# Performance work log

Hardware: AMD Instinct MI355X
Metric: run time of the kernel (lower is better)

## Reference

```python
import jax, jax.numpy as jnp
import numpy as np

NUM_HEADS = 16
NUM_KV_HEADS = 8
FEATURES = 3584
HEAD_DIM = 256
QUERY_SCALAR = 0.0625  # 1/sqrt(head_dim)
SOFT_CAP = 50.0
WINDOW = 1024
K_MASK = -2.3819763e+38
B, T = 1, 2048


def apply_rope(x, positions, head_dim, max_wavelength=10000):
    # x: [B,T,N,H], positions: [B,T]
    fraction = 2.0 * jnp.arange(head_dim // 2, dtype=jnp.float32) / head_dim
    timescale = max_wavelength ** fraction  # [H/2]
    sinusoid = positions[..., None].astype(jnp.float32) / timescale  # [B,T,H/2]
    sinusoid = sinusoid[..., None, :]  # [B,T,1,H/2]
    sin, cos = jnp.sin(sinusoid), jnp.cos(sinusoid)
    first, second = jnp.split(x, 2, axis=-1)
    return jnp.concatenate([first * cos - second * sin, second * cos + first * sin], axis=-1).astype(x.dtype)


def sliding_mask(segment_pos, window, cache_len):
    # cache=None prefill path: total_tokens == cache_len, cache_positions = arange
    cp = jnp.arange(cache_len)[None, None, :]      # [1,1,S]
    sp = segment_pos[:, :, None]                   # [B,T,1]
    return (cp > sp - window) & (cp < sp + window)  # [B,T,S]


def setup_inputs() -> dict:
    key = jax.random.key(0)
    k1, k2, k3, k4 = jax.random.split(key, 4)
    x = jax.random.normal(k1, (B, T, FEATURES), jnp.float32)
    wq = jax.random.normal(k2, (NUM_HEADS, FEATURES, HEAD_DIM), jnp.float32) * 0.02
    wkv = jax.random.normal(k3, (2, NUM_KV_HEADS, FEATURES, HEAD_DIM), jnp.float32) * 0.02
    wo = jax.random.normal(k4, (NUM_HEADS, HEAD_DIM, FEATURES), jnp.float32) * 0.02
    segment_pos = jnp.broadcast_to(jnp.arange(T, dtype=jnp.int32)[None, :], (B, T))
    attn_mask = jnp.broadcast_to(jnp.tril(jnp.ones((T, T), bool))[None], (B, T, T))
    return {"x": x, "segment_pos": segment_pos, "attn_mask": attn_mask, "wq": wq, "wkv": wkv, "wo": wo}


def reference(x, segment_pos, attn_mask, wq, wkv, wo):
    # Projections (GQA path: num_kv_heads != num_heads)
    q = jnp.einsum('BTD,NDH->BTNH', x, wq)            # [B,T,N,H]
    k, v = jnp.einsum('BSD,CKDH->CBSKH', x, wkv)      # each [B,S,K,H]
    q = apply_rope(q, segment_pos, HEAD_DIM) * QUERY_SCALAR
    k = apply_rope(k, segment_pos, HEAD_DIM)
    b, t, n, h = q.shape
    g = n // NUM_KV_HEADS
    qg = q.reshape(b, t, NUM_KV_HEADS, g, h)
    logits = jnp.einsum('BTKGH,BSKH->BTKGS', qg, k).reshape(b, t, n, t)
    # logit soft-capping
    logits = jnp.tanh(logits / SOFT_CAP) * SOFT_CAP
    # sliding-window (LOCAL_SLIDING) combined with causal mask
    mask = attn_mask & sliding_mask(segment_pos, WINDOW, t)
    padded = jnp.where(mask[:, :, None, :], logits, K_MASK)
    probs = jax.nn.softmax(padded, axis=-1).astype(k.dtype)
    pg = probs.reshape(b, t, NUM_KV_HEADS, g, t)
    encoded = jnp.einsum('BTKGS,BSKH->BTKGH', pg, v).reshape(b, t, n, h)
    return jnp.einsum('BTNH,NHD->BTD', encoded, wo)
```

## Files before the change

### kernel.cpp

```cpp
#include <hip/hip_runtime.h>
#include <stdint.h>

typedef unsigned short u16;
typedef __attribute__((ext_vector_type(8))) short short8;
typedef __attribute__((ext_vector_type(4))) float f32x4;

#define SEQ    2048
#define FEAT   3584
#define NHEAD  16
#define HD     256
#define WSLOT  917504

static __device__ __forceinline__ float bf2f(u16 v){
  union { unsigned u; float f; } x; x.u = ((unsigned)v) << 16; return x.f;
}
static __device__ __forceinline__ u16 f2bf(float f){
  union { float f; unsigned u; } x; x.f = f;
  unsigned r = x.u + 0x7fffu + ((x.u >> 16) & 1u);
  return (u16)(r >> 16);
}

static __device__ __forceinline__ void gl_lds16(const u16* g, u16* l){
  __builtin_amdgcn_global_load_lds((const __attribute__((address_space(1))) void*)g,
                                   (__attribute__((address_space(3))) void*)l,
                                   16, 0, 0);
}

__global__ void k_conv_x(const float* __restrict__ x, u16* __restrict__ xb){
  int i = (blockIdx.x * 256 + threadIdx.x) * 4;
  float4 v = *(const float4*)(x + i);
  ushort4 o; o.x = f2bf(v.x); o.y = f2bf(v.y); o.z = f2bf(v.z); o.w = f2bf(v.w);
  *(ushort4*)(xb + i) = o;
}

__global__ void k_rope_tab(const int* __restrict__ sp, float* __restrict__ rc, float* __restrict__ rs){
  int idx = blockIdx.x * 256 + threadIdx.x;
  int t = idx >> 7, i = idx & 127;
  float ts = powf(10000.0f, (float)i * (1.0f / 128.0f));
  float ang = (float)sp[t] / ts;
  float s, c;
  sincosf(ang, &s, &c);
  rc[idx] = c; rs[idx] = s;
}

__global__ void k_tconv_f32(const float* __restrict__ src, u16* __restrict__ dst,
                            long sslot, long dslot, int sld, int dld){
  __shared__ u16 tile[64][68];
  src += (long)blockIdx.z * sslot;
  dst += (long)blockIdx.z * dslot;
  int r0 = blockIdx.y * 64, c0 = blockIdx.x * 64;
  int t = threadIdx.x, rr = t >> 4, cc = t & 15;
  #pragma unroll
  for (int p = 0; p < 4; p++){
    int r = rr + p * 16;
    float4 v = *(const float4*)(src + (size_t)(r0 + r) * sld + c0 + cc * 4);
    ushort4 o; o.x = f2bf(v.x); o.y = f2bf(v.y); o.z = f2bf(v.z); o.w = f2bf(v.w);
    *(ushort4*)&tile[r][cc * 4] = o;
  }
  __syncthreads();
  #pragma unroll
  for (int p = 0; p < 4; p++){
    int c = rr + p * 16;
    ushort4 o;
    o.x = tile[cc*4+0][c]; o.y = tile[cc*4+1][c]; o.z = tile[cc*4+2][c]; o.w = tile[cc*4+3][c];
    *(ushort4*)(dst + (size_t)(c0 + c) * dld + r0 + cc * 4) = o;
  }
}

__global__ void k_tconv_u16(const u16* __restrict__ src, u16* __restrict__ dst,
                            long sslot, long dslot, int sld, int dld){
  __shared__ u16 tile[64][68];
  src += (long)blockIdx.z * sslot;
  dst += (long)blockIdx.z * dslot;
  int r0 = blockIdx.y * 64, c0 = blockIdx.x * 64;
  int t = threadIdx.x, rr = t >> 4, cc = t & 15;
  #pragma unroll
  for (int p = 0; p < 4; p++){
    int r = rr + p * 16;
    ushort4 v = *(const ushort4*)(src + (size_t)(r0 + r) * sld + c0 + cc * 4);
    *(ushort4*)&tile[r][cc * 4] = v;
  }
  __syncthreads();
  #pragma unroll
  for (int p = 0; p < 4; p++){
    int c = rr + p * 16;
    ushort4 o;
    o.x = tile[cc*4+0][c]; o.y = tile[cc*4+1][c]; o.z = tile[cc*4+2][c]; o.w = tile[cc*4+3][c];
    *(ushort4*)(dst + (size_t)(c0 + c) * dld + r0 + cc * 4) = o;
  }
}

__global__ void k_rope(u16* __restrict__ q, u16* __restrict__ kk,
                       const float* __restrict__ rc, const float* __restrict__ rs){
  int idx = blockIdx.x * 256 + threadIdx.x;
  int i4 = idx & 31; int rest = idx >> 5;
  int slot = rest % 24; int t = rest / 24;
  u16* base; float sc;
  if (slot < 16){ base = q + (size_t)t * 4096 + slot * 256; sc = 0.0625f; }
  else { base = kk + (size_t)t * 2048 + (slot - 16) * 256; sc = 1.0f; }
  int i = i4 * 4;
  ushort4 a = *(ushort4*)(base + i);
  ushort4 b = *(ushort4*)(base + i + 128);
  float4 c = *(const float4*)(rc + t * 128 + i);
  float4 s = *(const float4*)(rs + t * 128 + i);
  ushort4 oa, ob; float x1, x2;
  x1 = bf2f(a.x); x2 = bf2f(b.x); oa.x = f2bf((x1*c.x - x2*s.x)*sc); ob.x = f2bf((x2*c.x + x1*s.x)*sc);
  x1 = bf2f(a.y); x2 = bf2f(b.y); oa.y = f2bf((x1*c.y - x2*s.y)*sc); ob.y = f2bf((x2*c.y + x1*s.y)*sc);
  x1 = bf2f(a.z); x2 = bf2f(b.z); oa.z = f2bf((x1*c.z - x2*s.z)*sc); ob.z = f2bf((x2*c.z + x1*s.z)*sc);
  x1 = bf2f(a.w); x2 = bf2f(b.w); oa.w = f2bf((x1*c.w - x2*s.w)*sc); ob.w = f2bf((x2*c.w + x1*s.w)*sc);
  *(ushort4*)(base + i) = oa;
  *(ushort4*)(base + i + 128) = ob;
}

template<int MODE>
__global__ __launch_bounds__(256)
void k_gemm(const u16* __restrict__ A, int Ktot,
            const u16* __restrict__ Bq, const u16* __restrict__ Bkv,
            u16* __restrict__ Cq, u16* __restrict__ Ck, u16* __restrict__ Cv,
            float* __restrict__ Cf)
{
  __shared__ __align__(16) u16 As[128 * 32];
  __shared__ __align__(16) u16 Bs[128 * 32];
  int tid = threadIdx.x;
  int ct = blockIdx.x, mt = blockIdx.y;
  int m0 = mt * 128;
  const u16* Bbase;
  u16* Cb = nullptr; int ldc = 0; long ccol0 = 0;
  if (MODE == 0){
    int slot = ct >> 1;
    long pan = (long)(ct & 1) * 128 * FEAT;
    if (slot < 16){ Bbase = Bq + (long)slot * WSLOT + pan; Cb = Cq; ldc = 4096; ccol0 = (long)ct * 128; }
    else {
      Bbase = Bkv + (long)(slot - 16) * WSLOT + pan;
      if (slot < 24){ Cb = Ck; ccol0 = (long)(ct - 32) * 128; }
      else          { Cb = Cv; ccol0 = (long)(ct - 48) * 128; }
      ldc = 2048;
    }
  } else {
    Bbase = Bq + (long)ct * 128 * 4096; ldc = FEAT; ccol0 = (long)ct * 128;
  }
  const int ld = Ktot;
  int lane = tid & 63, wv = tid >> 6;
  int wm = wv >> 1, wn = wv & 1;
  int l15 = lane & 15, lk = lane >> 4;
  const u16* ga = A + (size_t)(m0 + (tid >> 2)) * ld + (tid & 3) * 8;
  const u16* gb = Bbase + (size_t)(tid >> 2) * ld + (tid & 3) * 8;
  int aoff = (wm * 64 + l15) * 32 + lk * 8;
  int boff = (wn * 64 + l15) * 32 + lk * 8;
  f32x4 acc[4][4];
  #pragma unroll
  for (int i = 0; i < 4; i++)
    #pragma unroll
    for (int j = 0; j < 4; j++)
      acc[i][j] = (f32x4){0.f, 0.f, 0.f, 0.f};
  int nk = Ktot / 32;
  for (int kt = 0; kt < nk; kt++){
    __syncthreads();
    gl_lds16(ga,                    As + tid * 8);
    gl_lds16(ga + 64 * (size_t)ld,  As + 2048 + tid * 8);
    gl_lds16(gb,                    Bs + tid * 8);
    gl_lds16(gb + 64 * (size_t)ld,  Bs + 2048 + tid * 8);
    ga += 32; gb += 32;
    __syncthreads();
    short8 af[4], bfr[4];
    #pragma unroll
    for (int i = 0; i < 4; i++) af[i]  = *(const short8*)(As + aoff + i * 512);
    #pragma unroll
    for (int j = 0; j < 4; j++) bfr[j] = *(const short8*)(Bs + boff + j * 512);
    #pragma unroll
    for (int i = 0; i < 4; i++)
      #pragma unroll
      for (int j = 0; j < 4; j++)
        acc[i][j] = __builtin_amdgcn_mfma_f32_16x16x32_bf16(af[i], bfr[j], acc[i][j], 0, 0, 0);
  }
  #pragma unroll
  for (int i = 0; i < 4; i++)
    #pragma unroll
    for (int j = 0; j < 4; j++)
      #pragma unroll
      for (int r = 0; r < 4; r++){
        int trow = m0 + wm * 64 + i * 16 + lk * 4 + r;
        long tcol = ccol0 + wn * 64 + j * 16 + l15;
        if (MODE == 0) Cb[(size_t)trow * ldc + tcol] = f2bf(acc[i][j][r]);
        else           Cf[(size_t)trow * FEAT + tcol] = acc[i][j][r];
      }
}

__global__ __launch_bounds__(512)
void k_attn(const u16* __restrict__ qb, const u16* __restrict__ kb,
            const u16* __restrict__ vt, u16* __restrict__ enc)
{
  __shared__ __align__(16) u16 P[4][16][32];
  __shared__ float Dsum[8][16];
  int tid = threadIdx.x, lane = tid & 63, wv = tid >> 6;
  int strip = wv >> 1, half = wv & 1;
  int head = blockIdx.x >> 5, qt = blockIdx.x & 31;
  int q0 = qt * 64;
  int kvh = head >> 1;
  int l15 = lane & 15, lk = lane >> 4;
  short8 qf[8];
  {
    const u16* qrow = qb + (size_t)(q0 + strip * 16 + l15) * 4096 + head * 256 + lk * 8;
    #pragma unroll
    for (int c = 0; c < 8; c++) qf[c] = *(const short8*)(qrow + c * 32);
  }
  f32x4 acc[8];
  #pragma unroll
  for (int nf = 0; nf < 8; nf++) acc[nf] = (f32x4){0.f, 0.f, 0.f, 0.f};
  float dsum[4] = {0.f, 0.f, 0.f, 0.f};
  int s_lo = q0 - 1023; if (s_lo < 0) s_lo = 0; s_lo &= ~31;
  int s_hi = q0 + 63;
  const u16* kbase = kb + kvh * 256 + lk * 8;
  const u16* vbase = vt + (size_t)kvh * 256 * 2048 + (size_t)(half * 128 + l15) * 2048 + lk * 8;
  for (int s0 = s_lo; s0 <= s_hi; s0 += 32){
    f32x4 sacc = (f32x4){0.f, 0.f, 0.f, 0.f};
    const u16* krow = kbase + (size_t)(s0 + half * 16 + l15) * 2048;
    #pragma unroll
    for (int c = 0; c < 8; c++){
      short8 kf = *(const short8*)(krow + c * 32);
      sacc = __builtin_amdgcn_mfma_f32_16x16x32_bf16(qf[c], kf, sacc, 0, 0, 0);
    }
    int s_el = s0 + half * 16 + l15;
    int tb = q0 + strip * 16 + lk * 4;
    #pragma unroll
    for (int r = 0; r < 4; r++){
      int t = tb + r;
      float z = sacc[r] * 0.02f;
      z = fminf(fmaxf(z, -20.f), 20.f);
      float e2 = __expf(2.f * z);
      float p = __expf(50.f * (e2 - 1.f) / (e2 + 1.f));
      p = (s_el <= t && s_el > t - 1024) ? p : 0.f;
      dsum[r] += p;
      P[strip][lk * 4 + r][half * 16 + l15] = f2bf(p);
    }
    __syncthreads();
    short8 pf = *(const short8*)(&P[strip][l15][lk * 8]);
    const u16* vrow = vbase + s0;
    #pragma unroll
    for (int nf = 0; nf < 8; nf++){
      short8 vf = *(const short8*)(vrow + nf * 16 * 2048);
      acc[nf] = __builtin_amdgcn_mfma_f32_16x16x32_bf16(pf, vf, acc[nf], 0, 0, 0);
    }
    __syncthreads();
  }
  #pragma unroll
  for (int r = 0; r < 4; r++){
    float d = dsum[r];
    d += __shfl_xor(d, 1); d += __shfl_xor(d, 2);
    d += __shfl_xor(d, 4); d += __shfl_xor(d, 8);
    dsum[r] = d;
  }
  if (l15 == 0){
    #pragma unroll
    for (int r = 0; r < 4; r++) Dsum[wv][lk * 4 + r] = dsum[r];
  }
  __syncthreads();
  #pragma unroll
  for (int r = 0; r < 4; r++){
    int tl = lk * 4 + r;
    float inv = 1.f / (Dsum[strip * 2][tl] + Dsum[strip * 2 + 1][tl]);
    size_t orow = (size_t)(q0 + strip * 16 + tl) * 4096 + head * 256 + half * 128;
    #pragma unroll
    for (int nf = 0; nf < 8; nf++)
      enc[orow + nf * 16 + l15] = f2bf(acc[nf][r] * inv);
  }
}

extern "C" void kernel_launch(void* const* d_in, const int* in_sizes, int n_in,
                              void* d_out, int out_size, void* d_ws, size_t ws_size,
                              hipStream_t stream)
{
  (void)in_sizes; (void)n_in; (void)out_size; (void)ws_size;
  const float* x   = (const float*)d_in[0];
  const int*   sp  = (const int*)d_in[1];
  const float* wq  = (const float*)d_in[3];
  const float* wkv = (const float*)d_in[4];
  const float* wo  = (const float*)d_in[5];
  float* out = (float*)d_out;
  char* ws = (char*)d_ws;
  u16*  xb   = (u16*)(ws + 0);
  u16*  wqT  = (u16*)(ws + 14680064);
  u16*  wkvT = (u16*)(ws + 44040192);
  u16*  qb   = (u16*)(ws + 73400320);
  u16*  kb   = (u16*)(ws + 90177536);
  u16*  vraw = (u16*)(ws + 98566144);
  u16*  vt   = (u16*)(ws + 106954752);
  u16*  enc  = (u16*)(ws + 115343360);
  float* rc  = (float*)(ws + 132120576);
  float* rs  = (float*)(ws + 133169152);

  k_conv_x  <<<7168, 256, 0, stream>>>(x, xb);
  k_rope_tab<<<1024, 256, 0, stream>>>(sp, rc, rs);
  k_tconv_f32<<<dim3(4, 56, 16), 256, 0, stream>>>(wq,  wqT,  WSLOT, WSLOT, 256, 3584);
  k_tconv_f32<<<dim3(4, 56, 16), 256, 0, stream>>>(wkv, wkvT, WSLOT, WSLOT, 256, 3584);
  k_gemm<0> <<<dim3(64, 16), 256, 0, stream>>>(xb, FEAT, wqT, wkvT, qb, kb, vraw, nullptr);
  k_rope    <<<6144, 256, 0, stream>>>(qb, kb, rc, rs);
  k_tconv_u16<<<dim3(4, 32, 8), 256, 0, stream>>>(vraw, vt, 256, 524288, 2048, 2048);
  k_attn    <<<dim3(512), 512, 0, stream>>>(qb, kb, vt, enc);
  k_tconv_f32<<<dim3(56, 4, 16), 256, 0, stream>>>(wo, wqT , WSLOT, 256, 3584, 4096);
  k_gemm<1> <<<dim3(28, 16), 256, 0, stream>>>(enc, 4096, wqT , nullptr,
                                               nullptr, nullptr, nullptr, out);
}
```

Baseline: 764.0 us.

## Restructure attention with 32x32 MFMA, in-register P exchange, and split-KV waves

The attention kernel now uses 32x32x16 MFMA tiles, computing S^T so that probabilities stay in registers and are repacked through lane shuffles instead of an LDS round trip with per-tile barriers. Each block covers both query heads of one KV head across two 32-row query tiles, and the KV range is split between two wave groups whose partial outputs and denominators are combined through shared memory at the end. This removes per-iteration __syncthreads and raises MFMA efficiency. In exchange it uses many more accumulator registers, halves the grid to 256 blocks, and adds a final reduction step.

```diff
diff --git a/kernel.cpp b/kernel.cpp
--- a/kernel.cpp
+++ b/kernel.cpp
@@ -4,6 +4,7 @@
 typedef unsigned short u16;
 typedef __attribute__((ext_vector_type(8))) short short8;
 typedef __attribute__((ext_vector_type(4))) float f32x4;
+typedef __attribute__((ext_vector_type(16))) float f32x16;
 
 #define SEQ    2048
 #define FEAT   3584
@@ -18,6 +19,9 @@
   union { float f; unsigned u; } x; x.f = f;
   unsigned r = x.u + 0x7fffu + ((x.u >> 16) & 1u);
   return (u16)(r >> 16);
+}
+static __device__ __forceinline__ unsigned pk2(float a, float b){
+  return (unsigned)f2bf(a) | ((unsigned)f2bf(b) << 16);
 }
 
 static __device__ __forceinline__ void gl_lds16(const u16* g, u16* l){
@@ -186,83 +190,126 @@
       }
 }
 
-__global__ __launch_bounds__(512)
+__global__ __launch_bounds__(512, 2)
 void k_attn(const u16* __restrict__ qb, const u16* __restrict__ kb,
             const u16* __restrict__ vt, u16* __restrict__ enc)
 {
-  __shared__ __align__(16) u16 P[4][16][32];
-  __shared__ float Dsum[8][16];
-  int tid = threadIdx.x, lane = tid & 63, wv = tid >> 6;
-  int strip = wv >> 1, half = wv & 1;
-  int head = blockIdx.x >> 5, qt = blockIdx.x & 31;
-  int q0 = qt * 64;
-  int kvh = head >> 1;
-  int l15 = lane & 15, lk = lane >> 4;
-  short8 qf[8];
+  __shared__ float cmb[4][64][64];
+  __shared__ float drow[4][32];
+  int tid = threadIdx.x;
+  int wv = tid >> 6, lane = tid & 63;
+  int unit = wv & 3, split = wv >> 2;
+  int l31 = lane & 31, hi = lane >> 5;
+  int kvh = blockIdx.x & 7, qp = blockIdx.x >> 3;
+  int head = kvh * 2 + (unit >> 1);
+  int q0 = qp * 64 + (unit & 1) * 32;
+  int t = q0 + l31;
+
+  short8 qf[16];
   {
-    const u16* qrow = qb + (size_t)(q0 + strip * 16 + l15) * 4096 + head * 256 + lk * 8;
-    #pragma unroll
-    for (int c = 0; c < 8; c++) qf[c] = *(const short8*)(qrow + c * 32);
-  }
-  f32x4 acc[8];
-  #pragma unroll
-  for (int nf = 0; nf < 8; nf++) acc[nf] = (f32x4){0.f, 0.f, 0.f, 0.f};
-  float dsum[4] = {0.f, 0.f, 0.f, 0.f};
-  int s_lo = q0 - 1023; if (s_lo < 0) s_lo = 0; s_lo &= ~31;
-  int s_hi = q0 + 63;
-  const u16* kbase = kb + kvh * 256 + lk * 8;
-  const u16* vbase = vt + (size_t)kvh * 256 * 2048 + (size_t)(half * 128 + l15) * 2048 + lk * 8;
-  for (int s0 = s_lo; s0 <= s_hi; s0 += 32){
-    f32x4 sacc = (f32x4){0.f, 0.f, 0.f, 0.f};
-    const u16* krow = kbase + (size_t)(s0 + half * 16 + l15) * 2048;
-    #pragma unroll
-    for (int c = 0; c < 8; c++){
-      short8 kf = *(const short8*)(krow + c * 32);
-      sacc = __builtin_amdgcn_mfma_f32_16x16x32_bf16(qf[c], kf, sacc, 0, 0, 0);
-    }
-    int s_el = s0 + half * 16 + l15;
-    int tb = q0 + strip * 16 + lk * 4;
-    #pragma unroll
-    for (int r = 0; r < 4; r++){
-      int t = tb + r;
+    const u16* qrow = qb + (size_t)t * 4096 + head * 256 + hi * 8;
+    #pragma unroll
+    for (int kk = 0; kk < 16; kk++) qf[kk] = *(const short8*)(qrow + kk * 16);
+  }
+  f32x16 acc[8];
+  #pragma unroll
+  for (int nf = 0; nf < 8; nf++)
+    #pragma unroll
+    for (int r = 0; r < 16; r++) acc[nf][r] = 0.f;
+  float dsum = 0.f;
+
+  int tl = q0 > 1023 ? (q0 - 1023) >> 5 : 0;
+  int th = (q0 + 31) >> 5;
+  int hcnt = (th - tl + 2) >> 1;
+  int ti0 = split ? tl + hcnt : tl;
+  int ti1 = split ? th + 1 : tl + hcnt;
+
+  const u16* kcol = kb + (size_t)kvh * 256 + hi * 8;
+  const u16* vcol = vt + (size_t)kvh * 524288 + (size_t)l31 * 2048 + hi * 8;
+
+  for (int ti = ti0; ti < ti1; ti++){
+    int s0 = ti << 5;
+    const u16* kr = kcol + (size_t)(s0 + l31) * 2048;
+    f32x16 sacc;
+    #pragma unroll
+    for (int r = 0; r < 16; r++) sacc[r] = 0.f;
+    #pragma unroll
+    for (int kk = 0; kk < 16; kk++){
+      short8 kf = *(const short8*)(kr + kk * 16);
+      sacc = __builtin_amdgcn_mfma_f32_32x32x16_bf16(kf, qf[kk], sacc, 0, 0, 0);
+    }
+    float p[16];
+    #pragma unroll
+    for (int r = 0; r < 16; r++){
+      int s = s0 + (r & 3) + 8 * (r >> 2) + 4 * hi;
       float z = sacc[r] * 0.02f;
       z = fminf(fmaxf(z, -20.f), 20.f);
       float e2 = __expf(2.f * z);
-      float p = __expf(50.f * (e2 - 1.f) / (e2 + 1.f));
-      p = (s_el <= t && s_el > t - 1024) ? p : 0.f;
-      dsum[r] += p;
-      P[strip][lk * 4 + r][half * 16 + l15] = f2bf(p);
+      float pw = __expf(50.f * (e2 - 1.f) / (e2 + 1.f));
+      pw = (s <= t && s > t - 1024) ? pw : 0.f;
+      dsum += pw;
+      p[r] = pw;
+    }
+    #pragma unroll
+    for (int ks = 0; ks < 2; ks++){
+      unsigned A0 = pk2(p[8*ks+0], p[8*ks+1]);
+      unsigned A1 = pk2(p[8*ks+2], p[8*ks+3]);
+      unsigned B0 = pk2(p[8*ks+4], p[8*ks+5]);
+      unsigned B1 = pk2(p[8*ks+6], p[8*ks+7]);
+      unsigned xA0 = (unsigned)__shfl_xor((int)A0, 32);
+      unsigned xA1 = (unsigned)__shfl_xor((int)A1, 32);
+      unsigned xB0 = (unsigned)__shfl_xor((int)B0, 32);
+      unsigned xB1 = (unsigned)__shfl_xor((int)B1, 32);
+      union { unsigned u[4]; short8 v; } pa;
+      pa.u[0] = hi ? xB0 : A0;
+      pa.u[1] = hi ? xB1 : A1;
+      pa.u[2] = hi ? B0 : xA0;
+      pa.u[3] = hi ? B1 : xA1;
+      const u16* vr = vcol + s0 + ks * 16;
+      #pragma unroll
+      for (int nf = 0; nf < 8; nf++){
+        short8 vf = *(const short8*)(vr + (size_t)nf * 32 * 2048);
+        acc[nf] = __builtin_amdgcn_mfma_f32_32x32x16_bf16(pa.v, vf, acc[nf], 0, 0, 0);
+      }
+    }
+  }
+
+  if (split) cmb[unit][0][lane] = dsum;
+  __syncthreads();
+  if (!split){
+    dsum += cmb[unit][0][lane];
+    dsum += __shfl_xor(dsum, 32);
+    if (hi == 0) drow[unit][l31] = 1.f / dsum;
+  }
+  __syncthreads();
+  #pragma unroll
+  for (int hf = 0; hf < 2; hf++){
+    if (split){
+      #pragma unroll
+      for (int nf = 0; nf < 4; nf++)
+        #pragma unroll
+        for (int r = 0; r < 16; r++)
+          cmb[unit][nf * 16 + r][lane] = acc[hf * 4 + nf][r];
     }
     __syncthreads();
-    short8 pf = *(const short8*)(&P[strip][l15][lk * 8]);
-    const u16* vrow = vbase + s0;
-    #pragma unroll
-    for (int nf = 0; nf < 8; nf++){
-      short8 vf = *(const short8*)(vrow + nf * 16 * 2048);
-      acc[nf] = __builtin_amdgcn_mfma_f32_16x16x32_bf16(pf, vf, acc[nf], 0, 0, 0);
+    if (!split){
+      #pragma unroll
+      for (int nf = 0; nf < 4; nf++)
+        #pragma unroll
+        for (int r = 0; r < 16; r++)
+          acc[hf * 4 + nf][r] += cmb[unit][nf * 16 + r][lane];
     }
     __syncthreads();
   }
-  #pragma unroll
-  for (int r = 0; r < 4; r++){
-    float d = dsum[r];
-    d += __shfl_xor(d, 1); d += __shfl_xor(d, 2);
-    d += __shfl_xor(d, 4); d += __shfl_xor(d, 8);
-    dsum[r] = d;
-  }
-  if (l15 == 0){
-    #pragma unroll
-    for (int r = 0; r < 4; r++) Dsum[wv][lk * 4 + r] = dsum[r];
-  }
-  __syncthreads();
-  #pragma unroll
-  for (int r = 0; r < 4; r++){
-    int tl = lk * 4 + r;
-    float inv = 1.f / (Dsum[strip * 2][tl] + Dsum[strip * 2 + 1][tl]);
-    size_t orow = (size_t)(q0 + strip * 16 + tl) * 4096 + head * 256 + half * 128;
+  if (!split){
     #pragma unroll
     for (int nf = 0; nf < 8; nf++)
-      enc[orow + nf * 16 + l15] = f2bf(acc[nf][r] * inv);
+      #pragma unroll
+      for (int r = 0; r < 16; r++){
+        int trow = (r & 3) + 8 * (r >> 2) + 4 * hi;
+        float inv = drow[unit][trow];
+        enc[(size_t)(q0 + trow) * 4096 + head * 256 + nf * 32 + l31] = f2bf(acc[nf][r] * inv);
+      }
   }
 }
 
@@ -296,7 +343,7 @@
   k_gemm<0> <<<dim3(64, 16), 256, 0, stream>>>(xb, FEAT, wqT, wkvT, qb, kb, vraw, nullptr);
   k_rope    <<<6144, 256, 0, stream>>>(qb, kb, rc, rs);
   k_tconv_u16<<<dim3(4, 32, 8), 256, 0, stream>>>(vraw, vt, 256, 524288, 2048, 2048);
-  k_attn    <<<dim3(512), 512, 0, stream>>>(qb, kb, vt, enc);
+  k_attn    <<<dim3(256), 512, 0, stream>>>(qb, kb, vt, enc);
   k_tconv_f32<<<dim3(56, 4, 16), 256, 0, stream>>>(wo, wqT , WSLOT, 256, 3584, 4096);
   k_gemm<1> <<<dim3(28, 16), 256, 0, stream>>>(enc, 4096, wqT , nullptr,
                                                nullptr, nullptr, nullptr, out);
```

After: 664.1 us. 1.15x faster.
